# Kernel optimization log

Measured on AMD Instinct MI355X. Metric: run time of the kernel, lower is better.

## Reference

```python
import jax, jax.numpy as jnp
import numpy as np

H = 4  # attention heads


def _lstm(x, Wih, Whh, b, reverse=False):
    # x: [N, L, din] -> hidden sequence [N, L, dh]; PyTorch gate order i,f,g,o
    if reverse:
        x = x[:, ::-1, :]
    xT = jnp.swapaxes(x, 0, 1)  # [L, N, din]
    dh = Whh.shape[1]
    N = x.shape[0]

    def step(carry, xt):
        h, c = carry
        z = xt @ Wih.T + h @ Whh.T + b
        i, f, g, o = jnp.split(z, 4, axis=-1)
        c = jax.nn.sigmoid(f) * c + jax.nn.sigmoid(i) * jnp.tanh(g)
        h = jax.nn.sigmoid(o) * jnp.tanh(c)
        return (h, c), h

    h0 = jnp.zeros((N, dh), x.dtype)
    _, hs = jax.lax.scan(step, (h0, h0), xT)
    hs = jnp.swapaxes(hs, 0, 1)
    if reverse:
        hs = hs[:, ::-1, :]
    return hs


def setup_inputs() -> dict:
    key = jax.random.key(0)
    ks = jax.random.split(key, 24)
    B, T, D = 8, 128, 512
    C, L, U, V, E = 1000, 8, 16, 5000, 256

    def w(k, shape, fan_in):
        return jax.random.normal(k, shape, jnp.float32) * (1.0 / np.sqrt(fan_in))

    inp = {
        'model_embed': jax.random.normal(ks[0], (B, T, D), jnp.float32),
        'emb_table': w(ks[1], (V, E), E),
        'ctx_Wih_f': w(ks[2], (4 * E, E), E),
        'ctx_Whh_f': w(ks[3], (4 * E, E), E),
        'ctx_b_f': jnp.zeros((4 * E,), jnp.float32),
        'ctx_Wih_b': w(ks[4], (4 * E, E), E),
        'ctx_Whh_b': w(ks[5], (4 * E, E), E),
        'ctx_b_b': jnp.zeros((4 * E,), jnp.float32),
        'ctx_out_W': w(ks[6], (D, 2 * E), 2 * E),
        'hist_Wih': w(ks[7], (4 * D, D), D),
        'hist_Whh': w(ks[8], (4 * D, D), D),
        'hist_b': jnp.zeros((4 * D,), jnp.float32),
        'hist_out_W': w(ks[9], (D, D), D),
        'Wq': w(ks[10], (D, D), D),
        'Wk': w(ks[11], (D, D), D),
        'Wv': w(ks[12], (D, D), D),
        'Wo': w(ks[13], (D, D), D),
        'acoustic_W': w(ks[14], (D, D), D),
        'context_idxs': jax.random.randint(ks[15], (C, L), 0, V),
        'context_history_idx': jax.random.randint(ks[16], (B, U), 0, C),
        'context_ilens': jax.random.randint(ks[17], (C,), 1, L + 1),
        'context_history_ilens': jax.random.randint(ks[18], (B,), 1, U + 1),
    }
    return inp


def reference(model_embed, emb_table, ctx_Wih_f, ctx_Whh_f, ctx_b_f,
              ctx_Wih_b, ctx_Whh_b, ctx_b_b, ctx_out_W,
              hist_Wih, hist_Whh, hist_b, hist_out_W,
              Wq, Wk, Wv, Wo, acoustic_W,
              context_idxs, context_history_idx, context_ilens,
              context_history_ilens):
    C, L = context_idxs.shape
    B, T, D = model_embed.shape
    U = context_history_idx.shape[1]

    # --- ContextEncoderBiLSTM: embed -> BiLSTM -> proj -> length-masked mean ---
    emb = emb_table[context_idxs]                               # [C, L, E]
    hf = _lstm(emb, ctx_Wih_f, ctx_Whh_f, ctx_b_f)
    hb = _lstm(emb, ctx_Wih_b, ctx_Whh_b, ctx_b_b, reverse=True)
    seq = jnp.concatenate([hf, hb], -1) @ ctx_out_W.T           # [C, L, D]
    m = (jnp.arange(L)[None, :] < context_ilens[:, None]).astype(seq.dtype)
    ctx_mean = (seq * m[..., None]).sum(1) / context_ilens[:, None].astype(seq.dtype)  # [C, D]

    # --- history gather + ContextHistoryEncoderLSTM ---
    hist_in = ctx_mean[context_history_idx.reshape(-1)].reshape(B, U, D)
    hist = _lstm(hist_in, hist_Wih, hist_Whh, hist_b) @ hist_out_W.T  # [B, U, D]

    # --- fuse acoustic + history, attention-based adapter ---
    mp = model_embed @ acoustic_W.T                             # [B, T, D]
    fused = (mp[:, :, None, :] + hist[:, None, :, :]).reshape(B, T * U, D)
    dh = D // H
    q = (fused @ Wq.T).reshape(B, T * U, H, dh)
    k = (ctx_mean @ Wk.T).reshape(C, H, dh)
    v = (ctx_mean @ Wv.T).reshape(C, H, dh)
    scores = jnp.einsum('bqhd,chd->bhqc', q, k) / jnp.sqrt(jnp.asarray(dh, q.dtype))
    attn = jax.nn.softmax(scores, axis=-1)                      # [B, H, TU, C]
    out = (jnp.einsum('bhqc,chd->bqhd', attn, v).reshape(B, T * U, D) @ Wo.T)
    out = out.reshape(B, T, U, D)
    prob = attn.reshape(B, H, T, U, C).mean(1)                  # [B, T, U, C]
    logit = scores.reshape(B, H, T, U, C).mean(1)

    # --- batch greedy monotonic decoding (scan over T, full length) ---
    probT = jnp.moveaxis(prob, 1, 0)                            # [T, B, U, C]
    outT = jnp.moveaxis(out, 1, 0)                              # [T, B, U, D]
    b_idx = jnp.arange(B)

    def step(u, inp):
        p_t, o_t = inp
        u_c = jnp.minimum(u, U - 1)
        valid_u = jnp.minimum(u + 1, U - 1)
        tok = context_history_idx[b_idx, valid_u]
        blank_p = p_t[b_idx, u_c, 0]
        tok_p = p_t[b_idx, u_c, tok]
        upd = (tok_p > blank_p).astype(jnp.int32)
        return u_c + upd, (u_c, o_t[b_idx, u_c])

    u0 = jnp.zeros((B,), jnp.int32)
    _, (idx, o) = jax.lax.scan(step, u0, (probT, outT))
    o = jnp.moveaxis(o, 0, 1)                                   # [B, T, D]
    return o, logit, prob
```

## Files before the change

kernel.cpp:

```cpp
#include <hip/hip_runtime.h>
#include <math.h>

namespace {
constexpr int B_ = 8, T_ = 128, D_ = 512, C_ = 1000, L_ = 8, U_ = 16, E_ = 256, H_ = 4;
constexpr int VOC_ = 5000;
constexpr int DH_ = D_ / H_;
constexpr int E4_ = 4 * E_;
constexpr int D4_ = 4 * D_;
constexpr int TU_ = T_ * U_;
constexpr int HC_ = H_ * C_;
constexpr float SCALE_ = 0.088388347648318447f;

constexpr int XZ_NB  = E4_ / 64;
constexpr int XZ_MB  = (VOC_ + 63) / 64;
constexpr int XZ_NWG = XZ_NB * XZ_MB;
constexpr int XZ_CPX = XZ_NWG / 8;

constexpr size_t XZ_    = 0;
constexpr size_t SM_    = 0;
constexpr size_t SH_    = SM_ + (size_t)B_ * T_ * HC_;
constexpr size_t AOUT_  = SH_ + (size_t)B_ * U_ * HC_;
constexpr size_t PVP_   = AOUT_ + (size_t)B_ * T_ * D_;
constexpr size_t REG_A  = 2ul * VOC_ * E4_;
constexpr size_t HPING  = REG_A;
constexpr size_t CST    = HPING + 2ul * C_ * E_;
constexpr size_t HPONG  = CST + 2ul * C_ * E_;
constexpr size_t HFALL  = HPONG + 2ul * C_ * E_;
constexpr size_t HBALL  = HFALL + (size_t)C_ * L_ * E_;
constexpr size_t CATM   = HBALL + (size_t)C_ * L_ * E_;
constexpr size_t CTXM   = CATM + (size_t)C_ * 2 * E_;
constexpr size_t KWS    = CTXM + (size_t)C_ * D_;
constexpr size_t VWS    = KWS + (size_t)C_ * D_;
constexpr size_t WQA    = VWS + (size_t)C_ * D_;
constexpr size_t WQH    = WQA + (size_t)D_ * D_;
constexpr size_t HXP    = WQH + (size_t)D_ * D_;
constexpr size_t HALL   = HXP + (size_t)B_ * U_ * D4_;
constexpr size_t HGLOB  = HALL + (size_t)B_ * U_ * D_;
constexpr size_t HG2    = HGLOB + (size_t)B_ * D_;
constexpr size_t HISTC  = HG2 + (size_t)B_ * D_;
constexpr size_t QM_    = HISTC + (size_t)B_ * D_;
constexpr size_t QH_    = QM_ + (size_t)B_ * T_ * D_;
constexpr size_t SMSUM  = QH_ + (size_t)B_ * U_ * D_;
constexpr size_t SHSUM  = SMSUM + (size_t)B_ * T_ * C_;
constexpr size_t DEN_   = SHSUM + (size_t)B_ * U_ * C_;
constexpr size_t BITS_  = DEN_ + (size_t)B_ * T_ * U_ * H_;
constexpr size_t USEL_  = BITS_ + 4096;
constexpr size_t WS_NEED = USEL_ + (size_t)B_ * T_;
}

__device__ __forceinline__ float fsig(float x)  { return 1.f / (1.f + __expf(-x)); }
__device__ __forceinline__ float ftanh(float x) { return 1.f - 2.f / (__expf(2.f * x) + 1.f); }
__device__ __forceinline__ void fma4(float4& a, float w, const float4& v) {
  a.x += w * v.x; a.y += w * v.y; a.z += w * v.z; a.w += w * v.w;
}

struct GemmP {
  const float* A1; int lda1;
  const int* ridx; int ridx_stride; int ridx_off;
  const float* W1; int ldw1;
  const float* bias;
  float* out; int ldc;
  int M, N, K;
  float scale;
  int a_zoff, w_zoff, c_zoff;
};

template <int TN>
__device__ __forceinline__ void gemm_core(const GemmP& g, int z, int by, int bx) {
  constexpr int UN = TN / 16;
  constexpr int WP = TN / 64;
  __shared__ float As[16][68];
  __shared__ float Ws[16][TN + 4];
  const int m0 = by * 64;
  const int n0 = bx * TN;
  if (m0 >= g.M || n0 >= g.N) return;
  const float* A1 = g.A1 + (long)z * g.a_zoff;
  const float* W1 = g.W1 + (long)z * g.w_zoff;
  float* out = g.out + (long)z * g.c_zoff;
  const int tid = threadIdx.x;
  const int tx = tid & 15, ty = tid >> 4;
  const int sr = tid >> 2, skq = (tid & 3) * 4;
  float acc[4][UN] = {};
  int sarow = -1;
  {
    const int gm = m0 + sr;
    if (gm < g.M) sarow = g.ridx ? g.ridx[gm * g.ridx_stride + g.ridx_off] : gm;
  }
  float4 pa, pw[WP];
  {
    pa = make_float4(0.f, 0.f, 0.f, 0.f);
    if (sarow >= 0) pa = *(const float4*)&A1[(long)sarow * g.lda1 + skq];
#pragma unroll
    for (int p = 0; p < WP; ++p) {
      const int gn = n0 + sr + p * 64;
      pw[p] = make_float4(0.f, 0.f, 0.f, 0.f);
      if (gn < g.N) pw[p] = *(const float4*)&W1[(long)gn * g.ldw1 + skq];
    }
  }
  for (int k0 = 0; k0 < g.K; k0 += 16) {
    As[skq][sr] = pa.x; As[skq + 1][sr] = pa.y; As[skq + 2][sr] = pa.z; As[skq + 3][sr] = pa.w;
#pragma unroll
    for (int p = 0; p < WP; ++p) {
      const int r = sr + p * 64;
      Ws[skq][r] = pw[p].x; Ws[skq + 1][r] = pw[p].y; Ws[skq + 2][r] = pw[p].z; Ws[skq + 3][r] = pw[p].w;
    }
    __syncthreads();
    const int kn = k0 + 16;
    if (kn < g.K) {
      pa = make_float4(0.f, 0.f, 0.f, 0.f);
      if (sarow >= 0) pa = *(const float4*)&A1[(long)sarow * g.lda1 + kn + skq];
#pragma unroll
      for (int p = 0; p < WP; ++p) {
        const int gn = n0 + sr + p * 64;
        pw[p] = make_float4(0.f, 0.f, 0.f, 0.f);
        if (gn < g.N) pw[p] = *(const float4*)&W1[(long)gn * g.ldw1 + kn + skq];
      }
    }
#pragma unroll
    for (int k = 0; k < 16; ++k) {
      const float4 a = *(const float4*)&As[k][ty * 4];
#pragma unroll
      for (int q = 0; q < UN / 4; ++q) {
        const float4 w = *(const float4*)&Ws[k][q * 64 + tx * 4];
        acc[0][q*4+0] += a.x * w.x; acc[0][q*4+1] += a.x * w.y; acc[0][q*4+2] += a.x * w.z; acc[0][q*4+3] += a.x * w.w;
        acc[1][q*4+0] += a.y * w.x; acc[1][q*4+1] += a.y * w.y; acc[1][q*4+2] += a.y * w.z; acc[1][q*4+3] += a.y * w.w;
        acc[2][q*4+0] += a.z * w.x; acc[2][q*4+1] += a.z * w.y; acc[2][q*4+2] += a.z * w.z; acc[2][q*4+3] += a.z * w.w;
        acc[3][q*4+0] += a.w * w.x; acc[3][q*4+1] += a.w * w.y; acc[3][q*4+2] += a.w * w.z; acc[3][q*4+3] += a.w * w.w;
      }
    }
    __syncthreads();
  }
#pragma unroll
  for (int i = 0; i < 4; ++i) {
    const int gm = m0 + ty * 4 + i;
    if (gm >= g.M) continue;
#pragma unroll
    for (int q = 0; q < UN / 4; ++q) {
#pragma unroll
      for (int j = 0; j < 4; ++j) {
        const int gn = n0 + q * 64 + tx * 4 + j;
        if (gn >= g.N) continue;
        float v2 = acc[i][q*4+j];
        if (g.bias) v2 += g.bias[gn];
        out[(long)gm * g.ldc + gn] = v2 * g.scale;
      }
    }
  }
}

__global__ __launch_bounds__(256) void k_gemm64(GemmP p)  { gemm_core<64>(p, blockIdx.z, blockIdx.y, blockIdx.x); }
__global__ __launch_bounds__(256) void k_gemm64x2(GemmP p0, GemmP p1, int zs) {
  int z = blockIdx.z;
  if (z < zs) gemm_core<64>(p0, z, blockIdx.y, blockIdx.x);
  else gemm_core<64>(p1, z - zs, blockIdx.y, blockIdx.x);
}
__global__ __launch_bounds__(256) void k_gemm64x3(GemmP p0, GemmP p1, GemmP p2) {
  int z = blockIdx.z;
  if (z == 0) gemm_core<64>(p0, 0, blockIdx.y, blockIdx.x);
  else if (z == 1) gemm_core<64>(p1, 0, blockIdx.y, blockIdx.x);
  else gemm_core<64>(p2, 0, blockIdx.y, blockIdx.x);
}
__global__ __launch_bounds__(256) void k_gemm128x2(GemmP p0, GemmP p1, int zs) {
  int z = blockIdx.z;
  if (z < zs) gemm_core<128>(p0, z, blockIdx.y, blockIdx.x);
  else gemm_core<128>(p1, z - zs, blockIdx.y, blockIdx.x);
}
__global__ __launch_bounds__(256) void k_gemm64xcd(GemmP p0, GemmP p1) {
  const int bid = blockIdx.x;
  const int logical = (bid & 7) * XZ_CPX + (bid >> 3);
  const int bx = logical % XZ_NB;
  const int by = logical / XZ_NB;
  if (blockIdx.z == 0) gemm_core<64>(p0, 0, by, bx);
  else gemm_core<64>(p1, 0, by, bx);
}

__global__ __launch_bounds__(256) void k_gemm_nn(
    const float* __restrict__ A0, const float* __restrict__ B0, float* __restrict__ O0,
    const float* __restrict__ A1, const float* __restrict__ B1, float* __restrict__ O1) {
  const float* A = blockIdx.z ? A1 : A0;
  const float* B = blockIdx.z ? B1 : B0;
  float* O = blockIdx.z ? O1 : O0;
  __shared__ float As[16][68];
  __shared__ float Bs[16][68];
  const int m0 = blockIdx.y * 64, n0 = blockIdx.x * 64;
  const int tid = threadIdx.x;
  const int tx = tid & 15, ty = tid >> 4;
  const int sr = tid >> 2, skq = (tid & 3) * 4;
  float acc[4][4] = {};
  for (int k0 = 0; k0 < 512; k0 += 16) {
    {
      float4 v = *(const float4*)&A[(long)(m0 + sr) * 512 + k0 + skq];
      As[skq][sr] = v.x; As[skq + 1][sr] = v.y; As[skq + 2][sr] = v.z; As[skq + 3][sr] = v.w;
    }
#pragma unroll
    for (int p = 0; p < 4; ++p) {
      int idx = tid + p * 256;
      int kk = idx >> 6, jj = idx & 63;
      Bs[kk][jj] = B[(long)(k0 + kk) * 512 + n0 + jj];
    }
    __syncthreads();
#pragma unroll
    for (int k = 0; k < 16; ++k) {
      const float4 a = *(const float4*)&As[k][ty * 4];
      const float4 w = *(const float4*)&Bs[k][tx * 4];
      acc[0][0] += a.x * w.x; acc[0][1] += a.x * w.y; acc[0][2] += a.x * w.z; acc[0][3] += a.x * w.w;
      acc[1][0] += a.y * w.x; acc[1][1] += a.y * w.y; acc[1][2] += a.y * w.z; acc[1][3] += a.y * w.w;
      acc[2][0] += a.z * w.x; acc[2][1] += a.z * w.y; acc[2][2] += a.z * w.z; acc[2][3] += a.z * w.w;
      acc[3][0] += a.w * w.x; acc[3][1] += a.w * w.y; acc[3][2] += a.w * w.z; acc[3][3] += a.w * w.w;
    }
    __syncthreads();
  }
#pragma unroll
  for (int i = 0; i < 4; ++i)
#pragma unroll
    for (int j = 0; j < 4; ++j)
      O[(long)(m0 + ty * 4 + i) * 512 + n0 + tx * 4 + j] = acc[i][j];
}

__global__ __launch_bounds__(256) void k_ctx_step(
    const float* __restrict__ xz, const int* __restrict__ ctx_idxs,
    const float* __restrict__ Whh_f, const float* __restrict__ Whh_b,
    const float* __restrict__ h_prev, float* __restrict__ h_next,
    float* __restrict__ c_st,
    float* __restrict__ hf_all, float* __restrict__ hb_all, int t) {
  __shared__ float Hs[32][20];
  __shared__ float Wg[4][32][68];
  __shared__ float zb[4][16][68];
  const int e0 = blockIdx.x * 64;
  const int c0 = blockIdx.y * 16;
  const int dir = blockIdx.z;
  const int tid = threadIdx.x;
  const float* Whh = dir ? Whh_b : Whh_f;
  const float* hp = h_prev + (size_t)dir * C_ * E_;
  const int gp = tid >> 7;
  const int rem = tid & 127;
  const int cy = rem >> 4;
  const int ex = rem & 15;
  const bool hstage = (tid < 128);
  const int hcr = tid & 15, hkq = ((tid >> 4) & 7) * 4;
  const int hc = c0 + hcr;
  float4 acc4[2][2];
  acc4[0][0] = acc4[0][1] = acc4[1][0] = acc4[1][1] = make_float4(0.f, 0.f, 0.f, 0.f);
  float4 phv = make_float4(0.f, 0.f, 0.f, 0.f);
  float4 pwv[8];
  if (hstage && hc < C_) phv = *(const float4*)&hp[(size_t)hc * E_ + hkq];
#pragma unroll
  for (int p = 0; p < 8; ++p) {
    int idx = tid + p * 256;
    int ee = idx & 63, kq = ((idx >> 6) & 7) * 4, gg = idx >> 9;
    pwv[p] = *(const float4*)&Whh[(size_t)(gg * E_ + e0 + ee) * E_ + kq];
  }
  for (int k0 = 0; k0 < E_; k0 += 32) {
    if (hstage) {
      Hs[hkq][hcr] = phv.x; Hs[hkq + 1][hcr] = phv.y; Hs[hkq + 2][hcr] = phv.z; Hs[hkq + 3][hcr] = phv.w;
    }
#pragma unroll
    for (int p = 0; p < 8; ++p) {
      int idx = tid + p * 256;
      int ee = idx & 63, kq = ((idx >> 6) & 7) * 4, gg = idx >> 9;
      Wg[gg][kq][ee] = pwv[p].x; Wg[gg][kq + 1][ee] = pwv[p].y; Wg[gg][kq + 2][ee] = pwv[p].z; Wg[gg][kq + 3][ee] = pwv[p].w;
    }
    __syncthreads();
    const int kn = k0 + 32;
    if (kn < E_) {
      phv = make_float4(0.f, 0.f, 0.f, 0.f);
      if (hstage && hc < C_) phv = *(const float4*)&hp[(size_t)hc * E_ + kn + hkq];
#pragma unroll
      for (int p = 0; p < 8; ++p) {
        int idx = tid + p * 256;
        int ee = idx & 63, kq = ((idx >> 6) & 7) * 4, gg = idx >> 9;
        pwv[p] = *(const float4*)&Whh[(size_t)(gg * E_ + e0 + ee) * E_ + kn + kq];
      }
    }
#pragma unroll
    for (int kk = 0; kk < 32; ++kk) {
      const float a0 = Hs[kk][cy * 2];
      const float a1 = Hs[kk][cy * 2 + 1];
#pragma unroll
      for (int gg = 0; gg < 2; ++gg) {
        const float4 w = *(const float4*)&Wg[gp * 2 + gg][kk][ex * 4];
        fma4(acc4[gg][0], a0, w);
        fma4(acc4[gg][1], a1, w);
      }
    }
    __syncthreads();
  }
#pragma unroll
  for (int gg = 0; gg < 2; ++gg) {
    *(float4*)&zb[gp * 2 + gg][cy * 2 + 0][ex * 4] = acc4[gg][0];
    *(float4*)&zb[gp * 2 + gg][cy * 2 + 1][ex * 4] = acc4[gg][1];
  }
  __syncthreads();
  const int lpos = dir ? (L_ - 1 - t) : t;
  const float* xz_dir = xz + (size_t)dir * VOC_ * E4_;
  float* c_state = c_st + (size_t)dir * C_ * E_;
  float* hn_out = h_next + (size_t)dir * C_ * E_;
  float* hall = dir ? hb_all : hf_all;
  const int oc = tid >> 4, oe = (tid & 15) * 4;
  const int c = c0 + oc;
  if (c < C_) {
    const int e = e0 + oe;
    const int tok = ctx_idxs[c * L_ + lpos];
    const float* xr = xz_dir + (size_t)tok * E4_;
    float zi[4], zf[4], zg[4], zo[4], cp[4], cn[4], hn[4];
    *(float4*)zi = *(const float4*)&xr[e];
    *(float4*)zf = *(const float4*)&xr[E_ + e];
    *(float4*)zg = *(const float4*)&xr[2 * E_ + e];
    *(float4*)zo = *(const float4*)&xr[3 * E_ + e];
    *(float4*)cp = *(const float4*)&c_state[(size_t)c * E_ + e];
#pragma unroll
    for (int j = 0; j < 4; ++j) {
      float vi = zi[j] + zb[0][oc][oe + j];
      float vf = zf[j] + zb[1][oc][oe + j];
      float vg = zg[j] + zb[2][oc][oe + j];
      float vo = zo[j] + zb[3][oc][oe + j];
      cn[j] = fsig(vf) * cp[j] + fsig(vi) * ftanh(vg);
      hn[j] = fsig(vo) * ftanh(cn[j]);
    }
    *(float4*)&c_state[(size_t)c * E_ + e] = *(float4*)cn;
    *(float4*)&hn_out[(size_t)c * E_ + e] = *(float4*)hn;
    *(float4*)&hall[((size_t)c * L_ + lpos) * E_ + e] = *(float4*)hn;
  }
}

__global__ __launch_bounds__(256) void k_ctx_mean(
    const float* __restrict__ hf_all, const float* __restrict__ hb_all,
    const int* __restrict__ ilens, float* __restrict__ cat_mean) {
  int idx = blockIdx.x * 256 + threadIdx.x;
  if (idx >= C_ * 2 * E_) return;
  int c = idx / (2 * E_), e = idx - c * 2 * E_;
  const float* src = (e < E_) ? hf_all : hb_all;
  int ee = e & (E_ - 1);
  int il = ilens[c];
  float s = 0.f;
#pragma unroll
  for (int l = 0; l < L_; ++l)
    if (l < il) s += src[((size_t)c * L_ + l) * E_ + ee];
  cat_mean[idx] = s / (float)il;
}

__global__ __launch_bounds__(256) void k_hist_step2(
    const float* __restrict__ xproj, const float* __restrict__ Whh,
    const float* __restrict__ hprev, float* __restrict__ hcur,
    float* __restrict__ cstG, float* __restrict__ hall, int u) {
  __shared__ float Wl[32][516];
  __shared__ float hb[8][520];
  const int tid = threadIdx.x;
  const int e0 = blockIdx.x * 8;
  {
    int lr = tid >> 3, part = tid & 7;
    int g2 = lr >> 3, e2 = lr & 7;
    const float* src = Whh + (size_t)(g2 * D_ + e0 + e2) * D_;
#pragma unroll
    for (int i = 0; i < 16; ++i) {
      int k4 = part + i * 8;
      *(float4*)&Wl[lr][k4 * 4] = *(const float4*)&src[k4 * 4];
    }
  }
  {
    int b2 = tid >> 5, part = tid & 31;
#pragma unroll
    for (int i = 0; i < 4; ++i) {
      int k4 = part + i * 32;
      float4 v = make_float4(0.f, 0.f, 0.f, 0.f);
      if (u > 0) v = *(const float4*)&hprev[(size_t)b2 * D_ + k4 * 4];
      *(float4*)&hb[b2][k4 * 4] = v;
    }
  }
  __syncthreads();
  const int b = tid >> 5, g = (tid >> 3) & 3, e = tid & 7;
  const int lr = tid & 31;
  float dot = 0.f;
#pragma unroll 8
  for (int k4 = 0; k4 < 128; ++k4) {
    float4 w = *(const float4*)&Wl[lr][k4 * 4];
    float4 h4 = *(const float4*)&hb[b][k4 * 4];
    dot += w.x * h4.x + w.y * h4.y + w.z * h4.z + w.w * h4.w;
  }
  float z = dot + xproj[((size_t)b * U_ + u) * D4_ + g * D_ + e0 + e];
  const int l = tid & 63;
  const int base = (l & 32) | e;
  float zi = __shfl(z, base, 64);
  float zf = __shfl(z, base + 8, 64);
  float zg = __shfl(z, base + 16, 64);
  float zo = __shfl(z, base + 24, 64);
  if (g == 0) {
    float cp = (u > 0) ? cstG[(size_t)b * D_ + e0 + e] : 0.f;
    float cn = fsig(zf) * cp + fsig(zi) * ftanh(zg);
    cstG[(size_t)b * D_ + e0 + e] = cn;
    float hv = fsig(zo) * ftanh(cn);
    hcur[(size_t)b * D_ + e0 + e] = hv;
    hall[((size_t)b * U_ + u) * D_ + e0 + e] = hv;
  }
}

__global__ __launch_bounds__(256) void k_rowexp(
    float* __restrict__ Sm, float* __restrict__ Sh,
    float* __restrict__ SmS, float* __restrict__ ShS) {
  int row = blockIdx.x;
  float* base; float* sumo;
  if (row < B_ * T_) { base = Sm + (size_t)row * HC_; sumo = SmS + (size_t)row * C_; }
  else { int r2 = row - B_ * T_; base = Sh + (size_t)r2 * HC_; sumo = ShS + (size_t)r2 * C_; }
  int tid = threadIdx.x;
  for (int c = tid; c < C_; c += 256) {
    float s = base[c] + base[C_ + c] + base[2 * C_ + c] + base[3 * C_ + c];
    sumo[c] = 0.25f * s;
  }
  __syncthreads();
  int h = tid >> 6, lane = tid & 63;
  float* p = base + (size_t)h * C_;
  float mx = -1e30f;
  for (int c = lane; c < C_; c += 64) mx = fmaxf(mx, p[c]);
#pragma unroll
  for (int o = 32; o; o >>= 1) mx = fmaxf(mx, __shfl_xor(mx, o));
  for (int c = lane; c < C_; c += 64) p[c] = __expf(p[c] - mx);
}

__global__ __launch_bounds__(256) void k_den(
    const float* __restrict__ EM, const float* __restrict__ EH,
    float* __restrict__ den) {
  const int bt = blockIdx.x;
  const int b = bt >> 7;
  const int h = threadIdx.x >> 6, lane = threadIdx.x & 63;
  const float* emp = EM + ((size_t)bt * H_ + h) * C_;
  float em[16];
#pragma unroll
  for (int i = 0; i < 16; ++i) {
    int c = lane + i * 64;
    em[i] = (c < C_) ? emp[c] : 0.f;
  }
  for (int u = 0; u < U_; ++u) {
    const float* ehp = EH + (((size_t)b * U_ + u) * H_ + h) * C_;
    float s = 0.f;
#pragma unroll
    for (int i = 0; i < 16; ++i) {
      int c = lane + i * 64;
      if (c < C_) s += em[i] * ehp[c];
    }
#pragma unroll
    for (int o = 32; o; o >>= 1) s += __shfl_xor(s, o);
    if (lane == 0) den[((size_t)bt * U_ + u) * H_ + h] = s;
  }
}

__global__ __launch_bounds__(256) void k_plw(
    const float* __restrict__ EM, const float* __restrict__ EH,
    const float* __restrict__ SmS, const float* __restrict__ ShS,
    const float* __restrict__ den, const int* __restrict__ hidx,
    float* __restrict__ prob, float* __restrict__ logit,
    unsigned char* __restrict__ bits) {
  __shared__ float sEM[H_][1008];
  __shared__ float sSS[1000];
  __shared__ float sB[4], sT[4];
  const int bt = blockIdx.x >> 2;
  const int ug = blockIdx.x & 3;
  const int b = bt >> 7;
  const int tid = threadIdx.x;
  for (int i = tid; i < H_ * C_; i += 256) sEM[i / C_][i % C_] = EM[(size_t)bt * HC_ + i];
  for (int c = tid; c < C_; c += 256) sSS[c] = SmS[(size_t)bt * C_ + c];
  __syncthreads();
#pragma unroll
  for (int j = 0; j < 4; ++j) {
    const int u = ug * 4 + j;
    const int valid = (u + 1 < U_ - 1) ? (u + 1) : (U_ - 1);
    const int tok = hidx[b * U_ + valid];
    const float* dnp = den + ((size_t)bt * U_ + u) * H_;
    const float i0 = 0.25f / dnp[0], i1 = 0.25f / dnp[1];
    const float i2 = 0.25f / dnp[2], i3 = 0.25f / dnp[3];
    const float* eh0 = EH + ((size_t)b * U_ + u) * HC_;
    const float* shs = ShS + ((size_t)b * U_ + u) * C_;
    size_t obase = ((size_t)bt * U_ + u) * C_;
    for (int c = tid; c < C_; c += 256) {
      float pr = sEM[0][c] * eh0[c] * i0 + sEM[1][c] * eh0[C_ + c] * i1
               + sEM[2][c] * eh0[2 * C_ + c] * i2 + sEM[3][c] * eh0[3 * C_ + c] * i3;
      __builtin_nontemporal_store(pr, &prob[obase + c]);
      __builtin_nontemporal_store(sSS[c] + shs[c], &logit[obase + c]);
      if (c == 0) sB[j] = pr;
      if (c == tok) sT[j] = pr;
    }
  }
  __syncthreads();
  if (tid < 4) bits[bt * U_ + ug * 4 + tid] = (sT[tid] > sB[tid]) ? 1 : 0;
}

__global__ __launch_bounds__(64) void k_scan(
    const unsigned char* __restrict__ bits, int* __restrict__ u_sel) {
  __shared__ unsigned char sb[B_ * T_ * U_];
  int tid = threadIdx.x;
  for (int i = tid; i < B_ * T_ * U_; i += 64) sb[i] = bits[i];
  __syncthreads();
  if (tid < B_) {
    int u = 0;
    for (int t = 0; t < T_; ++t) {
      int uc = (u < U_ - 1) ? u : (U_ - 1);
      u_sel[tid * T_ + t] = uc;
      u = uc + (int)sb[(tid * T_ + t) * U_ + uc];
    }
  }
}

__global__ __launch_bounds__(256) void k_pvg2(
    const float* __restrict__ EM, const float* __restrict__ EH,
    const float* __restrict__ den, const int* __restrict__ u_sel,
    const float* __restrict__ vmat, float* __restrict__ pvp) {
  constexpr int KC = 64;
  __shared__ float wS[2][4][4][KC + 4];
  __shared__ float invS[8][4];
  __shared__ int bS[8], tS[8], uS[8];
  const int tid = threadIdx.x;
  const int cblk = blockIdx.y;
  if (tid < 32) {
    int g8 = tid >> 2, hh = tid & 3;
    int bt = blockIdx.x * 8 + g8;
    int b = bt >> 7, t = bt & 127;
    int u = u_sel[bt];
    if (hh == 0) { bS[g8] = b; tS[g8] = t; uS[g8] = u; }
    invS[g8][hh] = 1.f / den[((size_t)bt * U_ + u) * H_ + hh];
  }
  __syncthreads();
  const int sub = tid >> 7, lt = tid & 127;
  const int d = lt * 4;
  const int h = lt >> 5;
  float4 acc[4];
  acc[0] = acc[1] = acc[2] = acc[3] = make_float4(0.f, 0.f, 0.f, 0.f);
  const int cbeg = cblk * 128;
  const int cend = (cbeg + 128 < C_) ? (cbeg + 128) : C_;
  for (int c0 = cbeg; c0 < cend; c0 += KC) {
#pragma unroll
    for (int p = 0; p < 8; ++p) {
      int idx = tid + p * 256;
      int cc = idx & 63;
      int rest = idx >> 6;
      int hh = rest & 3, gg = (rest >> 2) & 3, ss = rest >> 4;
      int g8 = ss * 4 + gg;
      int c = c0 + cc;
      float w = 0.f;
      if (c < C_) {
        int b = bS[g8], t = tS[g8], u = uS[g8];
        float em = EM[(((size_t)b * T_ + t) * H_ + hh) * C_ + c];
        float eh = EH[(((size_t)b * U_ + u) * H_ + hh) * C_ + c];
        w = em * eh * invS[g8][hh];
      }
      wS[ss][gg][hh][cc] = w;
    }
    __syncthreads();
#pragma unroll 4
    for (int q = 0; q < KC / 4; ++q) {
      const float4 w0 = *(const float4*)&wS[sub][0][h][q * 4];
      const float4 w1 = *(const float4*)&wS[sub][1][h][q * 4];
      const float4 w2 = *(const float4*)&wS[sub][2][h][q * 4];
      const float4 w3 = *(const float4*)&wS[sub][3][h][q * 4];
      int c = c0 + q * 4;
      float4 v;
      if (c < C_) { v = *(const float4*)&vmat[(size_t)c * D_ + d];
        fma4(acc[0], w0.x, v); fma4(acc[1], w1.x, v); fma4(acc[2], w2.x, v); fma4(acc[3], w3.x, v); }
      if (c + 1 < C_) { v = *(const float4*)&vmat[(size_t)(c + 1) * D_ + d];
        fma4(acc[0], w0.y, v); fma4(acc[1], w1.y, v); fma4(acc[2], w2.y, v); fma4(acc[3], w3.y, v); }
      if (c + 2 < C_) { v = *(const float4*)&vmat[(size_t)(c + 2) * D_ + d];
        fma4(acc[0], w0.z, v); fma4(acc[1], w1.z, v); fma4(acc[2], w2.z, v); fma4(acc[3], w3.z, v); }
      if (c + 3 < C_) { v = *(const float4*)&vmat[(size_t)(c + 3) * D_ + d];
        fma4(acc[0], w0.w, v); fma4(acc[1], w1.w, v); fma4(acc[2], w2.w, v); fma4(acc[3], w3.w, v); }
    }
    __syncthreads();
  }
  float* pout = pvp + (size_t)cblk * (B_ * T_) * D_;
#pragma unroll
  for (int g = 0; g < 4; ++g) {
    int bt = (bS[sub * 4 + g] << 7) + tS[sub * 4 + g];
    *(float4*)&pout[(size_t)bt * D_ + d] = acc[g];
  }
}

__global__ __launch_bounds__(256) void k_pvred(
    const float* __restrict__ pvp, float* __restrict__ aout) {
  const size_t i = ((size_t)blockIdx.x * 256 + threadIdx.x) * 4;
  float4 s = *(const float4*)&pvp[i];
#pragma unroll
  for (int k = 1; k < 8; ++k) {
    const float4 v = *(const float4*)&pvp[(size_t)k * (B_ * T_) * D_ + i];
    s.x += v.x; s.y += v.y; s.z += v.z; s.w += v.w;
  }
  *(float4*)&aout[i] = s;
}

extern "C" void kernel_launch(void* const* d_in, const int* in_sizes, int n_in,
                              void* d_out, int out_size, void* d_ws, size_t ws_size,
                              hipStream_t stream) {
  const float* model_embed = (const float*)d_in[0];
  const float* emb_table   = (const float*)d_in[1];
  const float* Wih_f = (const float*)d_in[2];
  const float* Whh_f = (const float*)d_in[3];
  const float* b_f   = (const float*)d_in[4];
  const float* Wih_b = (const float*)d_in[5];
  const float* Whh_b = (const float*)d_in[6];
  const float* b_b   = (const float*)d_in[7];
  const float* ctx_out_W  = (const float*)d_in[8];
  const float* hist_Wih   = (const float*)d_in[9];
  const float* hist_Whh   = (const float*)d_in[10];
  const float* hist_b     = (const float*)d_in[11];
  const float* hist_out_W = (const float*)d_in[12];
  const float* Wq = (const float*)d_in[13];
  const float* Wk = (const float*)d_in[14];
  const float* Wv = (const float*)d_in[15];
  const float* Wo = (const float*)d_in[16];
  const float* acoustic_W = (const float*)d_in[17];
  const int* ctx_idxs = (const int*)d_in[18];
  const int* hidx     = (const int*)d_in[19];
  const int* ilens    = (const int*)d_in[20];

  if (ws_size < WS_NEED * sizeof(float)) return;

  float* ws = (float*)d_ws;
  float* o_out     = (float*)d_out;
  float* logit_out = o_out + (size_t)B_ * T_ * D_;
  float* prob_out  = logit_out + (size_t)B_ * T_ * U_ * C_;

  hipMemsetAsync(ws + HPING, 0, 4ul * C_ * E_ * sizeof(float), stream);

  k_gemm_nn<<<dim3(8, 8, 2), 256, 0, stream>>>(
      Wq, acoustic_W, ws + WQA, Wq, hist_out_W, ws + WQH);

  {
    GemmP pf{};
    pf.A1 = emb_table; pf.lda1 = E_;
    pf.W1 = Wih_f; pf.ldw1 = E_;
    pf.bias = b_f;
    pf.out = ws + XZ_; pf.ldc = E4_;
    pf.M = VOC_; pf.N = E4_; pf.K = E_; pf.scale = 1.f;
    GemmP pb = pf;
    pb.W1 = Wih_b; pb.bias = b_b; pb.out = ws + XZ_ + (size_t)VOC_ * E4_;
    k_gemm64xcd<<<dim3(XZ_NWG, 1, 2), 256, 0, stream>>>(pf, pb);
  }

  for (int t = 0; t < L_; ++t) {
    float* hp = ws + ((t & 1) ? HPONG : HPING);
    float* hn = ws + ((t & 1) ? HPING : HPONG);
    k_ctx_step<<<dim3(4, (C_ + 15) / 16, 2), 256, 0, stream>>>(
        ws + XZ_, ctx_idxs, Whh_f, Whh_b, hp, hn, ws + CST,
        ws + HFALL, ws + HBALL, t);
  }

  k_ctx_mean<<<dim3((C_ * 2 * E_ + 255) / 256), 256, 0, stream>>>(
      ws + HFALL, ws + HBALL, ilens, ws + CATM);
  {
    GemmP p{};
    p.A1 = ws + CATM; p.lda1 = 2 * E_;
    p.W1 = ctx_out_W; p.ldw1 = 2 * E_;
    p.out = ws + CTXM; p.ldc = D_; p.M = C_; p.N = D_; p.K = 2 * E_; p.scale = 1.f;
    k_gemm64<<<dim3(8, 16, 1), 256, 0, stream>>>(p);
  }

  {
    GemmP pk{};
    pk.A1 = ws + CTXM; pk.lda1 = D_;
    pk.W1 = Wk; pk.ldw1 = D_;
    pk.out = ws + KWS; pk.ldc = D_; pk.M = C_; pk.N = D_; pk.K = D_; pk.scale = SCALE_;
    GemmP pv = pk;
    pv.W1 = Wv; pv.out = ws + VWS; pv.scale = 1.f;
    GemmP ph{};
    ph.A1 = ws + CTXM; ph.lda1 = D_;
    ph.ridx = hidx; ph.ridx_stride = 1; ph.ridx_off = 0;
    ph.W1 = hist_Wih; ph.ldw1 = D_;
    ph.bias = hist_b;
    ph.out = ws + HXP; ph.ldc = D4_; ph.M = B_ * U_; ph.N = D4_; ph.K = D_; ph.scale = 1.f;
    k_gemm64x3<<<dim3(32, 16, 3), 256, 0, stream>>>(pk, pv, ph);
  }

  for (int u = 0; u < U_; ++u) {
    const float* hp = ws + ((u & 1) ? HG2 : HGLOB);
    float* hc = ws + ((u & 1) ? HGLOB : HG2);
    k_hist_step2<<<dim3(64), 256, 0, stream>>>(
        ws + HXP, hist_Whh, hp, hc, ws + HISTC, ws + HALL, u);
  }

  {
    GemmP pm{};
    pm.A1 = model_embed; pm.lda1 = D_;
    pm.W1 = ws + WQA; pm.ldw1 = D_;
    pm.out = ws + QM_; pm.ldc = D_; pm.M = B_ * T_; pm.N = D_; pm.K = D_; pm.scale = 1.f;
    GemmP ph = pm;
    ph.A1 = ws + HALL; ph.W1 = ws + WQH; ph.out = ws + QH_; ph.M = B_ * U_;
    k_gemm64x2<<<dim3(8, 16, 2), 256, 0, stream>>>(pm, ph, 1);
  }

  {
    GemmP pm{};
    pm.A1 = ws + QM_; pm.lda1 = D_;
    pm.W1 = ws + KWS; pm.ldw1 = D_;
    pm.out = ws + SM_; pm.ldc = HC_; pm.M = B_ * T_; pm.N = C_; pm.K = DH_; pm.scale = 1.f;
    pm.a_zoff = DH_; pm.w_zoff = DH_; pm.c_zoff = C_;
    GemmP ph = pm;
    ph.A1 = ws + QH_; ph.out = ws + SH_; ph.M = B_ * U_;
    k_gemm128x2<<<dim3(8, 16, 8), 256, 0, stream>>>(pm, ph, 4);
  }

  k_rowexp<<<dim3(B_ * T_ + B_ * U_), 256, 0, stream>>>(
      ws + SM_, ws + SH_, ws + SMSUM, ws + SHSUM);

  k_den<<<dim3(B_ * T_), 256, 0, stream>>>(ws + SM_, ws + SH_, ws + DEN_);

  k_plw<<<dim3(B_ * T_ * 4), 256, 0, stream>>>(
      ws + SM_, ws + SH_, ws + SMSUM, ws + SHSUM, ws + DEN_, hidx,
      prob_out, logit_out, (unsigned char*)(ws + BITS_));

  k_scan<<<dim3(1), 64, 0, stream>>>((const unsigned char*)(ws + BITS_), (int*)(ws + USEL_));

  k_pvg2<<<dim3(128, 8), 256, 0, stream>>>(
      ws + SM_, ws + SH_, ws + DEN_, (const int*)(ws + USEL_), ws + VWS, ws + PVP_);
  k_pvred<<<dim3((B_ * T_ * D_) / (256 * 4)), 256, 0, stream>>>(ws + PVP_, ws + AOUT_);

  {
    GemmP p{};
    p.A1 = ws + AOUT_; p.lda1 = D_;
    p.W1 = Wo; p.ldw1 = D_;
    p.out = o_out; p.ldc = D_; p.M = B_ * T_; p.N = D_; p.K = D_; p.scale = 1.f;
    k_gemm64<<<dim3(8, 16, 1), 256, 0, stream>>>(p);
  }
}
```

Measured before the change: 776.6 us.

## Skip inactive forward-LSTM rows via length-sorted permutation; fuse denominator into plw

Adds a kernel that sorts context rows by length so the forward context LSTM step processes only rows still within their valid length at each timestep, with whole blocks exiting early. This relies on rows past their length never being read downstream. It also removes the separate k_den kernel and computes the per-head softmax denominators inside k_plw with a block reduction. The change saves a launch and an extra read of EM, but adds syncs per u iteration inside k_plw.

```diff
diff --git a/kernel.cpp b/kernel.cpp
--- a/kernel.cpp
+++ b/kernel.cpp
@@ -45,7 +45,9 @@
 constexpr size_t DEN_   = SHSUM + (size_t)B_ * U_ * C_;
 constexpr size_t BITS_  = DEN_ + (size_t)B_ * T_ * U_ * H_;
 constexpr size_t USEL_  = BITS_ + 4096;
-constexpr size_t WS_NEED = USEL_ + (size_t)B_ * T_;
+constexpr size_t PERM_  = USEL_ + (size_t)B_ * T_;
+constexpr size_t NACT_  = PERM_ + C_;
+constexpr size_t WS_NEED = NACT_ + 8;
 }
 
 __device__ __forceinline__ float fsig(float x)  { return 1.f / (1.f + __expf(-x)); }
@@ -217,18 +219,55 @@
       O[(long)(m0 + ty * 4 + i) * 512 + n0 + tx * 4 + j] = acc[i][j];
 }
 
+__global__ __launch_bounds__(256) void k_perm(
+    const int* __restrict__ ilens, int* __restrict__ perm, int* __restrict__ nact) {
+  __shared__ int cnt[9];
+  __shared__ int start[9];
+  const int tid = threadIdx.x;
+  if (tid < 9) cnt[tid] = 0;
+  __syncthreads();
+  for (int c = tid; c < C_; c += 256) atomicAdd(&cnt[ilens[c]], 1);
+  __syncthreads();
+  if (tid == 0) {
+    int acc = 0;
+    for (int k = 8; k >= 0; --k) { start[k] = acc; if (k > 0) acc += cnt[k]; }
+    for (int t = 0; t < 8; ++t) nact[t] = start[t];
+  }
+  __syncthreads();
+  const int wave = tid >> 6, lane = tid & 63;
+  for (int k = wave + 1; k <= 8; k += 4) {
+    int base = start[k];
+    for (int c0 = 0; c0 < C_; c0 += 64) {
+      int c = c0 + lane;
+      bool f = (c < C_) && (ilens[c] == k);
+      unsigned long long m = __ballot(f);
+      if (f) {
+        int r = __popcll(m & ((1ull << lane) - 1ull));
+        perm[base + r] = c;
+      }
+      base += __popcll(m);
+    }
+  }
+}
+
 __global__ __launch_bounds__(256) void k_ctx_step(
     const float* __restrict__ xz, const int* __restrict__ ctx_idxs,
     const float* __restrict__ Whh_f, const float* __restrict__ Whh_b,
     const float* __restrict__ h_prev, float* __restrict__ h_next,
     float* __restrict__ c_st,
-    float* __restrict__ hf_all, float* __restrict__ hb_all, int t) {
+    float* __restrict__ hf_all, float* __restrict__ hb_all,
+    const int* __restrict__ perm, const int* __restrict__ nactArr, int t) {
   __shared__ float Hs[32][20];
   __shared__ float Wg[4][32][68];
   __shared__ float zb[4][16][68];
   const int e0 = blockIdx.x * 64;
   const int c0 = blockIdx.y * 16;
   const int dir = blockIdx.z;
+  int nact = C_;
+  if (dir == 0) {
+    nact = nactArr[t];
+    if (c0 >= nact) return;
+  }
   const int tid = threadIdx.x;
   const float* Whh = dir ? Whh_b : Whh_f;
   const float* hp = h_prev + (size_t)dir * C_ * E_;
@@ -239,11 +278,14 @@
   const bool hstage = (tid < 128);
   const int hcr = tid & 15, hkq = ((tid >> 4) & 7) * 4;
   const int hc = c0 + hcr;
+  int hrow = -1;
+  if (dir == 0) { if (hc < nact) hrow = perm[hc]; }
+  else if (hc < C_) hrow = hc;
   float4 acc4[2][2];
   acc4[0][0] = acc4[0][1] = acc4[1][0] = acc4[1][1] = make_float4(0.f, 0.f, 0.f, 0.f);
   float4 phv = make_float4(0.f, 0.f, 0.f, 0.f);
   float4 pwv[8];
-  if (hstage && hc < C_) phv = *(const float4*)&hp[(size_t)hc * E_ + hkq];
+  if (hstage && hrow >= 0) phv = *(const float4*)&hp[(size_t)hrow * E_ + hkq];
 #pragma unroll
   for (int p = 0; p < 8; ++p) {
     int idx = tid + p * 256;
@@ -264,7 +306,7 @@
     const int kn = k0 + 32;
     if (kn < E_) {
       phv = make_float4(0.f, 0.f, 0.f, 0.f);
-      if (hstage && hc < C_) phv = *(const float4*)&hp[(size_t)hc * E_ + kn + hkq];
+      if (hstage && hrow >= 0) phv = *(const float4*)&hp[(size_t)hrow * E_ + kn + hkq];
 #pragma unroll
       for (int p = 0; p < 8; ++p) {
         int idx = tid + p * 256;
@@ -297,8 +339,11 @@
   float* hn_out = h_next + (size_t)dir * C_ * E_;
   float* hall = dir ? hb_all : hf_all;
   const int oc = tid >> 4, oe = (tid & 15) * 4;
-  const int c = c0 + oc;
-  if (c < C_) {
+  const int lc = c0 + oc;
+  int c = -1;
+  if (dir == 0) { if (lc < nact) c = perm[lc]; }
+  else if (lc < C_) c = lc;
+  if (c >= 0) {
     const int e = e0 + oe;
     const int tok = ctx_idxs[c * L_ + lpos];
     const float* xr = xz_dir + (size_t)tok * E4_;
@@ -416,42 +461,17 @@
   for (int c = lane; c < C_; c += 64) p[c] = __expf(p[c] - mx);
 }
 
-__global__ __launch_bounds__(256) void k_den(
-    const float* __restrict__ EM, const float* __restrict__ EH,
-    float* __restrict__ den) {
-  const int bt = blockIdx.x;
-  const int b = bt >> 7;
-  const int h = threadIdx.x >> 6, lane = threadIdx.x & 63;
-  const float* emp = EM + ((size_t)bt * H_ + h) * C_;
-  float em[16];
-#pragma unroll
-  for (int i = 0; i < 16; ++i) {
-    int c = lane + i * 64;
-    em[i] = (c < C_) ? emp[c] : 0.f;
-  }
-  for (int u = 0; u < U_; ++u) {
-    const float* ehp = EH + (((size_t)b * U_ + u) * H_ + h) * C_;
-    float s = 0.f;
-#pragma unroll
-    for (int i = 0; i < 16; ++i) {
-      int c = lane + i * 64;
-      if (c < C_) s += em[i] * ehp[c];
-    }
-#pragma unroll
-    for (int o = 32; o; o >>= 1) s += __shfl_xor(s, o);
-    if (lane == 0) den[((size_t)bt * U_ + u) * H_ + h] = s;
-  }
-}
-
 __global__ __launch_bounds__(256) void k_plw(
     const float* __restrict__ EM, const float* __restrict__ EH,
     const float* __restrict__ SmS, const float* __restrict__ ShS,
-    const float* __restrict__ den, const int* __restrict__ hidx,
-    float* __restrict__ prob, float* __restrict__ logit,
+    const int* __restrict__ hidx,
+    float* __restrict__ den, float* __restrict__ prob, float* __restrict__ logit,
     unsigned char* __restrict__ bits) {
   __shared__ float sEM[H_][1008];
   __shared__ float sSS[1000];
   __shared__ float sB[4], sT[4];
+  __shared__ float sW[4][4];
+  __shared__ float sInvU[4];
   const int bt = blockIdx.x >> 2;
   const int ug = blockIdx.x & 3;
   const int b = bt >> 7;
@@ -464,10 +484,29 @@
     const int u = ug * 4 + j;
     const int valid = (u + 1 < U_ - 1) ? (u + 1) : (U_ - 1);
     const int tok = hidx[b * U_ + valid];
-    const float* dnp = den + ((size_t)bt * U_ + u) * H_;
-    const float i0 = 0.25f / dnp[0], i1 = 0.25f / dnp[1];
-    const float i2 = 0.25f / dnp[2], i3 = 0.25f / dnp[3];
     const float* eh0 = EH + ((size_t)b * U_ + u) * HC_;
+    float d0 = 0.f, d1 = 0.f, d2 = 0.f, d3 = 0.f;
+    for (int c = tid; c < C_; c += 256) {
+      d0 += sEM[0][c] * eh0[c];
+      d1 += sEM[1][c] * eh0[C_ + c];
+      d2 += sEM[2][c] * eh0[2 * C_ + c];
+      d3 += sEM[3][c] * eh0[3 * C_ + c];
+    }
+#pragma unroll
+    for (int o = 32; o; o >>= 1) {
+      d0 += __shfl_xor(d0, o); d1 += __shfl_xor(d1, o);
+      d2 += __shfl_xor(d2, o); d3 += __shfl_xor(d3, o);
+    }
+    const int wv = tid >> 6;
+    if ((tid & 63) == 0) { sW[wv][0] = d0; sW[wv][1] = d1; sW[wv][2] = d2; sW[wv][3] = d3; }
+    __syncthreads();
+    if (tid < 4) {
+      float dd = sW[0][tid] + sW[1][tid] + sW[2][tid] + sW[3][tid];
+      den[((size_t)bt * U_ + u) * H_ + tid] = dd;
+      sInvU[tid] = 0.25f / dd;
+    }
+    __syncthreads();
+    const float i0 = sInvU[0], i1 = sInvU[1], i2 = sInvU[2], i3 = sInvU[3];
     const float* shs = ShS + ((size_t)b * U_ + u) * C_;
     size_t obase = ((size_t)bt * U_ + u) * C_;
     for (int c = tid; c < C_; c += 256) {
@@ -478,8 +517,8 @@
       if (c == 0) sB[j] = pr;
       if (c == tok) sT[j] = pr;
     }
-  }
-  __syncthreads();
+    __syncthreads();
+  }
   if (tid < 4) bits[bt * U_ + ug * 4 + tid] = (sT[tid] > sB[tid]) ? 1 : 0;
 }
 
@@ -617,6 +656,8 @@
 
   hipMemsetAsync(ws + HPING, 0, 4ul * C_ * E_ * sizeof(float), stream);
 
+  k_perm<<<dim3(1), 256, 0, stream>>>(ilens, (int*)(ws + PERM_), (int*)(ws + NACT_));
+
   k_gemm_nn<<<dim3(8, 8, 2), 256, 0, stream>>>(
       Wq, acoustic_W, ws + WQA, Wq, hist_out_W, ws + WQH);
 
@@ -637,7 +678,8 @@
     float* hn = ws + ((t & 1) ? HPING : HPONG);
     k_ctx_step<<<dim3(4, (C_ + 15) / 16, 2), 256, 0, stream>>>(
         ws + XZ_, ctx_idxs, Whh_f, Whh_b, hp, hn, ws + CST,
-        ws + HFALL, ws + HBALL, t);
+        ws + HFALL, ws + HBALL,
+        (const int*)(ws + PERM_), (const int*)(ws + NACT_), t);
   }
 
   k_ctx_mean<<<dim3((C_ * 2 * E_ + 255) / 256), 256, 0, stream>>>(
@@ -697,11 +739,9 @@
   k_rowexp<<<dim3(B_ * T_ + B_ * U_), 256, 0, stream>>>(
       ws + SM_, ws + SH_, ws + SMSUM, ws + SHSUM);
 
-  k_den<<<dim3(B_ * T_), 256, 0, stream>>>(ws + SM_, ws + SH_, ws + DEN_);
-
   k_plw<<<dim3(B_ * T_ * 4), 256, 0, stream>>>(
-      ws + SM_, ws + SH_, ws + SMSUM, ws + SHSUM, ws + DEN_, hidx,
-      prob_out, logit_out, (unsigned char*)(ws + BITS_));
+      ws + SM_, ws + SH_, ws + SMSUM, ws + SHSUM, hidx,
+      ws + DEN_, prob_out, logit_out, (unsigned char*)(ws + BITS_));
 
   k_scan<<<dim3(1), 64, 0, stream>>>((const unsigned char*)(ws + BITS_), (int*)(ws + USEL_));
 
```

Result: faster. 760.1 us (-2.1%).
